# Kernel optimization log

Hardware: AMD Instinct MI355X
Metric: run time of the kernel (lower is better)

The kernel has to match this reference:

```python
import jax, jax.numpy as jnp
import numpy as np

EMBED_DIM = 1024
NUM_HEADS = 16
HEAD_DIM = EMBED_DIM // NUM_HEADS
BATCH = 4
SEQ = 2048


def setup_inputs() -> dict:
    key = jax.random.key(0)
    ks = jax.random.split(key, 5)
    s_in = 1.0 / np.sqrt(EMBED_DIM)
    x = jax.random.normal(ks[0], (BATCH, SEQ, EMBED_DIM), dtype=jnp.float32)
    # torch nn.Linear params: weight [out, in], bias [out]
    qkv_w = jax.random.uniform(ks[1], (3 * EMBED_DIM, EMBED_DIM), jnp.float32, -s_in, s_in)
    qkv_b = jax.random.uniform(ks[2], (3 * EMBED_DIM,), jnp.float32, -s_in, s_in)
    out_w = jax.random.uniform(ks[3], (EMBED_DIM, EMBED_DIM), jnp.float32, -s_in, s_in)
    out_b = jax.random.uniform(ks[4], (EMBED_DIM,), jnp.float32, -s_in, s_in)
    return {"x": x, "qkv_w": qkv_w, "qkv_b": qkv_b, "out_w": out_w, "out_b": out_b}


def reference(x, qkv_w, qkv_b, out_w, out_b):
    B, S, E = x.shape
    qkv = x @ qkv_w.T + qkv_b                      # [B,S,3E]
    qkv = qkv.reshape(B, S, 3, NUM_HEADS, HEAD_DIM)
    qkv = jnp.transpose(qkv, (2, 0, 3, 1, 4))      # [3,B,H,S,D]
    q, k, v = qkv[0], qkv[1], qkv[2]
    scale = jnp.sqrt(jnp.float32(HEAD_DIM))
    scores = jnp.einsum('bhqd,bhkd->bhqk', q, k) / scale  # [B,H,S,S]
    attn = jax.nn.softmax(scores, axis=-1)
    out = jnp.einsum('bhqk,bhkd->bhqd', attn, v)   # [B,H,S,D]
    out = jnp.transpose(out, (0, 2, 1, 3)).reshape(B, S, E)
    return out @ out_w.T + out_b
```

## Files before the change

kernel.cpp:

```cpp
#include <hip/hip_runtime.h>
#include <hip/hip_bf16.h>

typedef _Float16 f16;
typedef __attribute__((ext_vector_type(8))) _Float16 f16x8;
typedef __attribute__((ext_vector_type(4))) _Float16 f16x4;
typedef __attribute__((ext_vector_type(4))) float f32x4;

#define MFMA16(a, b, c) __builtin_amdgcn_mfma_f32_16x16x32_f16(a, b, c, 0, 0, 0)
#define GLDS(src, dst) __builtin_amdgcn_global_load_lds( \
    (const __attribute__((address_space(1))) void*)(src), \
    (__attribute__((address_space(3))) void*)(dst), 16, 0, 0)

__device__ inline unsigned pkrtz(float a, float b) {
    __fp16 __attribute__((ext_vector_type(2))) r = __builtin_amdgcn_cvt_pkrtz(a, b);
    unsigned u; __builtin_memcpy(&u, &r, 4);
    return u;
}
__device__ inline void pl32swap(unsigned& a, unsigned& b) {
    asm volatile("v_permlane32_swap_b32 %0, %1" : "+v"(a), "+v"(b));
}
__device__ inline void pl16swap(unsigned& a, unsigned& b) {
    asm volatile("v_permlane16_swap_b32 %0, %1" : "+v"(a), "+v"(b));
}
__device__ inline float fexp2(float x) {
#if __has_builtin(__builtin_amdgcn_exp2f)
    return __builtin_amdgcn_exp2f(x);
#else
    return exp2f(x);
#endif
}

__global__ void cvt_all(const float4* __restrict__ x, const float4* __restrict__ qw,
                        const float4* __restrict__ ow,
                        f16x4* __restrict__ xo, f16x4* __restrict__ qwo,
                        f16x4* __restrict__ owo) {
    const int N1 = 2097152, N2 = 786432, N3 = 262144;
    int i = blockIdx.x * blockDim.x + threadIdx.x;
    int stride = gridDim.x * blockDim.x;
    for (; i < N1 + N2 + N3; i += stride) {
        const float4* src; f16x4* dst; int j;
        if (i < N1)            { src = x;  dst = xo;  j = i; }
        else if (i < N1 + N2)  { src = qw; dst = qwo; j = i - N1; }
        else                   { src = ow; dst = owo; j = i - N1 - N2; }
        float4 f = src[j];
        f16x4 h;
        h.x = (f16)f.x; h.y = (f16)f.y; h.z = (f16)f.z; h.w = (f16)f.w;
        dst[j] = h;
    }
}

__global__ __launch_bounds__(256, 2) void gemm_bt(
    const f16* __restrict__ A, const f16* __restrict__ Bw,
    const float* __restrict__ bias, int mode,
    f16* __restrict__ qo, f16* __restrict__ ko, f16* __restrict__ vo,
    float* __restrict__ outp)
{
    __shared__ __align__(16) f16 As[128 * 64];
    __shared__ __align__(16) f16 Bs[128 * 64];
    const int tid = threadIdx.x;
    const int wave = tid >> 6, lane = tid & 63;
    const int wr = wave >> 1, wc = wave & 1;
    const int brow = blockIdx.y * 128;
    const int bcol = blockIdx.x * 128;
    const int K = 1024;
    const f16* Ab = A + (size_t)brow * K;
    const f16* Bb = Bw + (size_t)bcol * K;

    const f32x4 fz = {0.0f, 0.0f, 0.0f, 0.0f};
    f32x4 acc[4][4];
#pragma unroll
    for (int m = 0; m < 4; ++m)
#pragma unroll
        for (int n = 0; n < 4; ++n) acc[m][n] = fz;

    const int lrow = lane >> 3;
    const int lcol = (lane & 7) * 8;
    const int cl = lane & 15, rg = lane >> 4;

    for (int k0 = 0; k0 < K; k0 += 64) {
        __syncthreads();
#pragma unroll
        for (int c = 0; c < 4; ++c) {
            const int ch = wave * 4 + c;
            const f16* srcA = Ab + (size_t)(ch * 8 + lrow) * K + k0 + lcol;
            const f16* srcB = Bb + (size_t)(ch * 8 + lrow) * K + k0 + lcol;
            GLDS(srcA, As + ch * 512);
            GLDS(srcB, Bs + ch * 512);
        }
        __syncthreads();
#pragma unroll
        for (int kk = 0; kk < 2; ++kk) {
            f16x8 af[4], bfr[4];
#pragma unroll
            for (int m = 0; m < 4; ++m)
                af[m] = *(const f16x8*)(As + (wr * 64 + m * 16 + cl) * 64 + kk * 32 + rg * 8);
#pragma unroll
            for (int n = 0; n < 4; ++n)
                bfr[n] = *(const f16x8*)(Bs + (wc * 64 + n * 16 + cl) * 64 + kk * 32 + rg * 8);
#pragma unroll
            for (int m = 0; m < 4; ++m)
#pragma unroll
                for (int n = 0; n < 4; ++n)
                    acc[m][n] = MFMA16(af[m], bfr[n], acc[m][n]);
        }
    }

    if (mode == 0) {
#pragma unroll
        for (int n = 0; n < 4; ++n) {
            int col = bcol + wc * 64 + n * 16 + cl;
            float bs = bias[col];
            int which = col >> 10;
            int h = (col & 1023) >> 6;
            int d = col & 63;
            if (which == 2) {
#pragma unroll
                for (int m = 0; m < 4; ++m) {
                    int row0 = brow + wr * 64 + m * 16 + rg * 4;
                    int bb = row0 >> 11, s0 = row0 & 2047;
                    f16x4 pk;
#pragma unroll
                    for (int r = 0; r < 4; ++r) pk[r] = (f16)(acc[m][n][r] + bs);
                    *(f16x4*)(vo + ((size_t)(bb * 16 + h) * 64 + d) * 2048 + s0) = pk;
                }
            } else {
                f16* dst = (which == 0) ? qo : ko;
                float scale = (which == 0) ? 0.125f * 1.44269504f : 1.0f;
#pragma unroll
                for (int m = 0; m < 4; ++m) {
#pragma unroll
                    for (int r = 0; r < 4; ++r) {
                        int row = brow + wr * 64 + m * 16 + rg * 4 + r;
                        int bb = row >> 11, s = row & 2047;
                        dst[((size_t)(bb * 16 + h) * 2048 + s) * 64 + d] =
                            (f16)((acc[m][n][r] + bs) * scale);
                    }
                }
            }
        }
    } else {
#pragma unroll
        for (int n = 0; n < 4; ++n) {
            int col = bcol + wc * 64 + n * 16 + cl;
            float bs = bias[col];
#pragma unroll
            for (int m = 0; m < 4; ++m)
#pragma unroll
                for (int r = 0; r < 4; ++r) {
                    int row = brow + wr * 64 + m * 16 + rg * 4 + r;
                    outp[(size_t)row * 1024 + col] = acc[m][n][r] + bs;
                }
        }
    }
}

__global__ __launch_bounds__(256, 3) void attn_fwd(
    const f16* __restrict__ Q, const f16* __restrict__ Kg,
    const f16* __restrict__ Vtg, f16* __restrict__ Op, float* __restrict__ lp)
{
    const int bid = blockIdx.x;
    const int vid = (bid & 7) * 256 + (bid >> 3);
    const int qx = vid & 15;
    const int bh = (vid >> 4) & 63;
    const int z  = vid >> 10;
    const int q0 = qx * 128;
    const int kb = z * 1024;
    const int tid = threadIdx.x;
    const int wave = tid >> 6, lane = tid & 63;
    const int cl = lane & 15, rg = lane >> 4;
    const f16* Qh = Q + (size_t)bh * 2048 * 64;
    const f16* Kp = Kg + (size_t)bh * 2048 * 64 + (size_t)kb * 64;
    const f16* Vp = Vtg + (size_t)bh * 64 * 2048 + kb;

    __shared__ __align__(16) f16 Ks[2][64 * 64];
    __shared__ __align__(16) f16 Vs[2][64 * 64];

    f16x8 aq[2][2];
#pragma unroll
    for (int m = 0; m < 2; ++m) {
        const f16* qptr = Qh + (size_t)(q0 + wave * 32 + m * 16 + cl) * 64 + rg * 8;
        aq[m][0] = *(const f16x8*)(qptr);
        aq[m][1] = *(const f16x8*)(qptr + 32);
    }

    f16x8 ones8;
#pragma unroll
    for (int j = 0; j < 8; ++j) ones8[j] = (f16)1.0f;

    const int srow0 = tid >> 3;
    const int schunk = tid & 7;
    const int swz = cl & 7;

    const f32x4 fz = {0.0f, 0.0f, 0.0f, 0.0f};
    f32x4 oacc[2][4];
    f32x4 loacc[2];
#pragma unroll
    for (int m = 0; m < 2; ++m) {
        loacc[m] = fz;
#pragma unroll
        for (int da = 0; da < 4; ++da) oacc[m][da] = fz;
    }

#pragma unroll
    for (int c = 0; c < 2; ++c) {
        int row = c * 32 + srow0;
        int sc = (schunk ^ (row & 7)) * 8;
        GLDS(Kp + (size_t)row * 64 + sc,   &Ks[0][(c * 256 + wave * 64) * 8]);
        GLDS(Vp + (size_t)row * 2048 + sc, &Vs[0][(c * 256 + wave * 64) * 8]);
    }

    int cur = 0;
    for (int t = 0; t < 16; ++t) {
        if (t < 15) {
            const int kt = (t + 1) * 64;
#pragma unroll
            for (int c = 0; c < 2; ++c) {
                int row = c * 32 + srow0;
                int sc = (schunk ^ (row & 7)) * 8;
                GLDS(Kp + (size_t)(kt + row) * 64 + sc, &Ks[cur ^ 1][(c * 256 + wave * 64) * 8]);
                GLDS(Vp + (size_t)row * 2048 + kt + sc, &Vs[cur ^ 1][(c * 256 + wave * 64) * 8]);
            }
            asm volatile("s_waitcnt vmcnt(4)" ::: "memory");
        } else {
            asm volatile("s_waitcnt vmcnt(0)" ::: "memory");
        }
        __builtin_amdgcn_sched_barrier(0);
        __builtin_amdgcn_s_barrier();
        __builtin_amdgcn_sched_barrier(0);

        f32x4 sacc[2][4];
        __builtin_amdgcn_s_setprio(1);
#pragma unroll
        for (int fn = 0; fn < 4; ++fn) {
            f16x8 ak0 = *(const f16x8*)(
                &Ks[cur][(fn * 16 + cl) * 64 + (rg ^ swz) * 8]);
            f16x8 ak1 = *(const f16x8*)(
                &Ks[cur][(fn * 16 + cl) * 64 + ((4 | rg) ^ swz) * 8]);
            sacc[0][fn] = MFMA16(ak0, aq[0][0], fz);
            sacc[0][fn] = MFMA16(ak1, aq[0][1], sacc[0][fn]);
            sacc[1][fn] = MFMA16(ak0, aq[1][0], fz);
            sacc[1][fn] = MFMA16(ak1, aq[1][1], sacc[1][fn]);
        }
        __builtin_amdgcn_s_setprio(0);

        f16x8 pbv[2][2];
#pragma unroll
        for (int m = 0; m < 2; ++m) {
            unsigned X0[4], X1[4];
#pragma unroll
            for (int fn = 0; fn < 4; ++fn) {
                float p0 = fexp2(sacc[m][fn][0]);
                float p1 = fexp2(sacc[m][fn][1]);
                float p2 = fexp2(sacc[m][fn][2]);
                float p3 = fexp2(sacc[m][fn][3]);
                X0[fn] = pkrtz(p0, p1);
                X1[fn] = pkrtz(p2, p3);
            }
#pragma unroll
            for (int kk = 0; kk < 2; ++kk) {
                unsigned a0 = X0[2 * kk], b0 = X0[2 * kk + 1];
                unsigned a1 = X1[2 * kk], b1 = X1[2 * kk + 1];
                pl32swap(a0, b0); pl16swap(a0, b0);
                pl32swap(a1, b1); pl16swap(a1, b1);
                unsigned fr[4] = {a0, a1, b0, b1};
                __builtin_memcpy(&pbv[m][kk], fr, 16);
            }
        }

        __builtin_amdgcn_s_setprio(1);
#pragma unroll
        for (int kk = 0; kk < 2; ++kk) {
            loacc[0] = MFMA16(ones8, pbv[0][kk], loacc[0]);
            loacc[1] = MFMA16(ones8, pbv[1][kk], loacc[1]);
#pragma unroll
            for (int da = 0; da < 4; ++da) {
                f16x8 av = *(const f16x8*)(
                    &Vs[cur][(da * 16 + cl) * 64 + (((kk << 2) | rg) ^ swz) * 8]);
                oacc[0][da] = MFMA16(av, pbv[0][kk], oacc[0][da]);
                oacc[1][da] = MFMA16(av, pbv[1][kk], oacc[1][da]);
            }
        }
        __builtin_amdgcn_s_setprio(0);

        asm volatile("s_waitcnt lgkmcnt(0)" ::: "memory");
        __builtin_amdgcn_sched_barrier(0);
        __builtin_amdgcn_s_barrier();
        __builtin_amdgcn_sched_barrier(0);
        cur ^= 1;
    }

    const int bb = bh >> 4, h = bh & 15;
#pragma unroll
    for (int m = 0; m < 2; ++m) {
        int s = q0 + wave * 32 + m * 16 + cl;
        int row = (bb * 2048 + s) * 16 + h;
        f16* op = Op + (size_t)z * 8388608 + (size_t)row * 64;
#pragma unroll
        for (int da = 0; da < 4; ++da) {
            f16x4 ov;
#pragma unroll
            for (int r = 0; r < 4; ++r) ov[r] = (f16)oacc[m][da][r];
            *(f16x4*)(op + da * 16 + rg * 4) = ov;
        }
        if (rg == 0) lp[z * 131072 + row] = loacc[m][0];
    }
}

__global__ __launch_bounds__(256) void attn_merge(
    const f16* __restrict__ Op, const float* __restrict__ lp, f16* __restrict__ AO)
{
    int i = blockIdx.x * 256 + threadIdx.x;
    int row = i >> 3, c = (i & 7) * 8;
    float inv = 1.0f / (lp[row] + lp[row + 131072]);
    f16x8 a = *(const f16x8*)(Op + (size_t)row * 64 + c);
    f16x8 b = *(const f16x8*)(Op + 8388608 + (size_t)row * 64 + c);
    f16x8 o;
#pragma unroll
    for (int j = 0; j < 8; ++j) o[j] = (f16)(((float)a[j] + (float)b[j]) * inv);
    *(f16x8*)(AO + (size_t)row * 64 + c) = o;
}

extern "C" void kernel_launch(void* const* d_in, const int* in_sizes, int n_in,
                              void* d_out, int out_size, void* d_ws, size_t ws_size,
                              hipStream_t stream) {
    const float* x     = (const float*)d_in[0];
    const float* qkv_w = (const float*)d_in[1];
    const float* qkv_b = (const float*)d_in[2];
    const float* out_w = (const float*)d_in[3];
    const float* out_b = (const float*)d_in[4];
    float* out = (float*)d_out;

    char* ws = (char*)d_ws;
    size_t off = 0;
    f16* x_h  = (f16*)(ws + off); off += 16777216;
    f16* qw_h = (f16*)(ws + off); off += 6291456;
    f16* ow_h = (f16*)(ws + off); off += 2097152;
    f16* Qb   = (f16*)(ws + off); off += 16777216;
    f16* Kb   = (f16*)(ws + off); off += 16777216;
    f16* Vb   = (f16*)(ws + off); off += 16777216;
    f16* AO   = (f16*)(ws + off); off += 16777216;
    f16* Opart= (f16*)(ws + off); off += 33554432;
    float* lpart = (float*)(ws + off); off += 1048576;

    cvt_all<<<2048, 256, 0, stream>>>((const float4*)x, (const float4*)qkv_w,
                                      (const float4*)out_w,
                                      (f16x4*)x_h, (f16x4*)qw_h, (f16x4*)ow_h);

    dim3 g1(24, 64);
    gemm_bt<<<g1, dim3(256), 0, stream>>>(x_h, qw_h, qkv_b, 0, Qb, Kb, Vb, nullptr);
    attn_fwd<<<2048, dim3(256), 0, stream>>>(Qb, Kb, Vb, Opart, lpart);
    attn_merge<<<4096, dim3(256), 0, stream>>>(Opart, lpart, AO);
    dim3 g2(8, 64);
    gemm_bt<<<g2, dim3(256), 0, stream>>>(AO, ow_h, out_b, 1, nullptr, nullptr, nullptr, out);
}
```

Before: 196.7 us.

## Use 256x256 double-buffered swizzled GEMM kernel for QKV projection

Replaces the 128x128 QKV projection GEMM with a dedicated 256x256-tile, 512-thread kernel. It double-buffers LDS with async global-to-LDS loads and manual vmcnt waits, XOR-swizzles LDS chunks to avoid bank conflicts, and raises wave priority around the MFMA block. The aim is more operand reuse per load and overlap of loads with compute. The cost is 128KB of LDS, one block per CU, and a smaller grid of 384 blocks that may leave CUs underfilled. The output-projection GEMM is split into its own kernel with unchanged logic.

```diff
diff --git a/kernel.cpp b/kernel.cpp
--- a/kernel.cpp
+++ b/kernel.cpp
@@ -49,11 +49,129 @@
     }
 }
 
-__global__ __launch_bounds__(256, 2) void gemm_bt(
+__global__ __launch_bounds__(512, 1) void gemm256_qkv(
     const f16* __restrict__ A, const f16* __restrict__ Bw,
-    const float* __restrict__ bias, int mode,
-    f16* __restrict__ qo, f16* __restrict__ ko, f16* __restrict__ vo,
-    float* __restrict__ outp)
+    const float* __restrict__ bias,
+    f16* __restrict__ qo, f16* __restrict__ ko, f16* __restrict__ vo)
+{
+    __shared__ __align__(16) f16 As[2][256 * 64];
+    __shared__ __align__(16) f16 Bs[2][256 * 64];
+    const int tid = threadIdx.x;
+    const int wave = tid >> 6, lane = tid & 63;
+    const int wr = wave >> 2, wc = wave & 3;
+    const int brow = blockIdx.y * 256;
+    const int bcol = blockIdx.x * 256;
+    const int K = 1024;
+    const f16* Ab = A + (size_t)brow * K;
+    const f16* Bb = Bw + (size_t)bcol * K;
+
+    const int cl = lane & 15, rg = lane >> 4;
+    const int swz = cl & 7;
+    const int schunk = tid & 7;
+
+    const f32x4 fz = {0.0f, 0.0f, 0.0f, 0.0f};
+    f32x4 acc[8][4];
+#pragma unroll
+    for (int m = 0; m < 8; ++m)
+#pragma unroll
+        for (int n = 0; n < 4; ++n) acc[m][n] = fz;
+
+#define STAGE(b, k0)                                                             \
+    {                                                                            \
+        _Pragma("unroll")                                                        \
+        for (int q = 0; q < 4; ++q) {                                            \
+            int id = q * 512 + tid;                                              \
+            int row = id >> 3;                                                   \
+            int sc = (schunk ^ (row & 7)) * 8;                                   \
+            GLDS(Ab + (size_t)row * 1024 + (k0) + sc, &As[b][id * 8 - lane * 8 + lane * 8]); \
+        }                                                                        \
+        _Pragma("unroll")                                                        \
+        for (int q = 0; q < 4; ++q) {                                            \
+            int id = q * 512 + tid;                                              \
+            int row = id >> 3;                                                   \
+            int sc = (schunk ^ (row & 7)) * 8;                                   \
+            GLDS(Bb + (size_t)row * 1024 + (k0) + sc, &Bs[b][id * 8]);           \
+        }                                                                        \
+    }
+
+    STAGE(0, 0);
+
+    int cur = 0;
+    for (int t = 0; t < 16; ++t) {
+        if (t < 15) {
+            STAGE(cur ^ 1, (t + 1) * 64);
+            asm volatile("s_waitcnt vmcnt(8)" ::: "memory");
+        } else {
+            asm volatile("s_waitcnt vmcnt(0)" ::: "memory");
+        }
+        __builtin_amdgcn_sched_barrier(0);
+        __builtin_amdgcn_s_barrier();
+        __builtin_amdgcn_sched_barrier(0);
+
+        __builtin_amdgcn_s_setprio(1);
+#pragma unroll
+        for (int kk = 0; kk < 2; ++kk) {
+            f16x8 af[8];
+#pragma unroll
+            for (int m = 0; m < 8; ++m)
+                af[m] = *(const f16x8*)(
+                    &As[cur][((wr * 128 + m * 16 + cl) * 8 + (((kk << 2) | rg) ^ swz)) * 8]);
+#pragma unroll
+            for (int n = 0; n < 4; ++n) {
+                f16x8 bf = *(const f16x8*)(
+                    &Bs[cur][((wc * 64 + n * 16 + cl) * 8 + (((kk << 2) | rg) ^ swz)) * 8]);
+#pragma unroll
+                for (int m = 0; m < 8; ++m)
+                    acc[m][n] = MFMA16(af[m], bf, acc[m][n]);
+            }
+        }
+        __builtin_amdgcn_s_setprio(0);
+
+        asm volatile("s_waitcnt lgkmcnt(0)" ::: "memory");
+        __builtin_amdgcn_sched_barrier(0);
+        __builtin_amdgcn_s_barrier();
+        __builtin_amdgcn_sched_barrier(0);
+        cur ^= 1;
+    }
+#undef STAGE
+
+#pragma unroll
+    for (int n = 0; n < 4; ++n) {
+        int col = bcol + wc * 64 + n * 16 + cl;
+        float bs = bias[col];
+        int which = col >> 10;
+        int h = (col & 1023) >> 6;
+        int d = col & 63;
+        if (which == 2) {
+#pragma unroll
+            for (int m = 0; m < 8; ++m) {
+                int row0 = brow + wr * 128 + m * 16 + rg * 4;
+                int bb = row0 >> 11, s0 = row0 & 2047;
+                f16x4 pk;
+#pragma unroll
+                for (int r = 0; r < 4; ++r) pk[r] = (f16)(acc[m][n][r] + bs);
+                *(f16x4*)(vo + ((size_t)(bb * 16 + h) * 64 + d) * 2048 + s0) = pk;
+            }
+        } else {
+            f16* dst = (which == 0) ? qo : ko;
+            float scale = (which == 0) ? 0.125f * 1.44269504f : 1.0f;
+#pragma unroll
+            for (int m = 0; m < 8; ++m) {
+#pragma unroll
+                for (int r = 0; r < 4; ++r) {
+                    int row = brow + wr * 128 + m * 16 + rg * 4 + r;
+                    int bb = row >> 11, s = row & 2047;
+                    dst[((size_t)(bb * 16 + h) * 2048 + s) * 64 + d] =
+                        (f16)((acc[m][n][r] + bs) * scale);
+                }
+            }
+        }
+    }
+}
+
+__global__ __launch_bounds__(256, 2) void gemm_out(
+    const f16* __restrict__ A, const f16* __restrict__ Bw,
+    const float* __restrict__ bias, float* __restrict__ outp)
 {
     __shared__ __align__(16) f16 As[128 * 64];
     __shared__ __align__(16) f16 Bs[128 * 64];
@@ -82,10 +200,8 @@
 #pragma unroll
         for (int c = 0; c < 4; ++c) {
             const int ch = wave * 4 + c;
-            const f16* srcA = Ab + (size_t)(ch * 8 + lrow) * K + k0 + lcol;
-            const f16* srcB = Bb + (size_t)(ch * 8 + lrow) * K + k0 + lcol;
-            GLDS(srcA, As + ch * 512);
-            GLDS(srcB, Bs + ch * 512);
+            GLDS(Ab + (size_t)(ch * 8 + lrow) * K + k0 + lcol, As + ch * 512);
+            GLDS(Bb + (size_t)(ch * 8 + lrow) * K + k0 + lcol, Bs + ch * 512);
         }
         __syncthreads();
 #pragma unroll
@@ -104,53 +220,17 @@
                     acc[m][n] = MFMA16(af[m], bfr[n], acc[m][n]);
         }
     }
-
-    if (mode == 0) {
-#pragma unroll
-        for (int n = 0; n < 4; ++n) {
-            int col = bcol + wc * 64 + n * 16 + cl;
-            float bs = bias[col];
-            int which = col >> 10;
-            int h = (col & 1023) >> 6;
-            int d = col & 63;
-            if (which == 2) {
-#pragma unroll
-                for (int m = 0; m < 4; ++m) {
-                    int row0 = brow + wr * 64 + m * 16 + rg * 4;
-                    int bb = row0 >> 11, s0 = row0 & 2047;
-                    f16x4 pk;
-#pragma unroll
-                    for (int r = 0; r < 4; ++r) pk[r] = (f16)(acc[m][n][r] + bs);
-                    *(f16x4*)(vo + ((size_t)(bb * 16 + h) * 64 + d) * 2048 + s0) = pk;
-                }
-            } else {
-                f16* dst = (which == 0) ? qo : ko;
-                float scale = (which == 0) ? 0.125f * 1.44269504f : 1.0f;
-#pragma unroll
-                for (int m = 0; m < 4; ++m) {
-#pragma unroll
-                    for (int r = 0; r < 4; ++r) {
-                        int row = brow + wr * 64 + m * 16 + rg * 4 + r;
-                        int bb = row >> 11, s = row & 2047;
-                        dst[((size_t)(bb * 16 + h) * 2048 + s) * 64 + d] =
-                            (f16)((acc[m][n][r] + bs) * scale);
-                    }
-                }
-            }
-        }
-    } else {
-#pragma unroll
-        for (int n = 0; n < 4; ++n) {
-            int col = bcol + wc * 64 + n * 16 + cl;
-            float bs = bias[col];
-#pragma unroll
-            for (int m = 0; m < 4; ++m)
-#pragma unroll
-                for (int r = 0; r < 4; ++r) {
-                    int row = brow + wr * 64 + m * 16 + rg * 4 + r;
-                    outp[(size_t)row * 1024 + col] = acc[m][n][r] + bs;
-                }
-        }
+#pragma unroll
+    for (int n = 0; n < 4; ++n) {
+        int col = bcol + wc * 64 + n * 16 + cl;
+        float bs = bias[col];
+#pragma unroll
+        for (int m = 0; m < 4; ++m)
+#pragma unroll
+            for (int r = 0; r < 4; ++r) {
+                int row = brow + wr * 64 + m * 16 + rg * 4 + r;
+                outp[(size_t)row * 1024 + col] = acc[m][n][r] + bs;
+            }
     }
 }
 
@@ -346,10 +426,10 @@
                                       (const float4*)out_w,
                                       (f16x4*)x_h, (f16x4*)qw_h, (f16x4*)ow_h);
 
-    dim3 g1(24, 64);
-    gemm_bt<<<g1, dim3(256), 0, stream>>>(x_h, qw_h, qkv_b, 0, Qb, Kb, Vb, nullptr);
+    dim3 g1(12, 32);
+    gemm256_qkv<<<g1, dim3(512), 0, stream>>>(x_h, qw_h, qkv_b, Qb, Kb, Vb);
     attn_fwd<<<2048, dim3(256), 0, stream>>>(Qb, Kb, Vb, Opart, lpart);
     attn_merge<<<4096, dim3(256), 0, stream>>>(Opart, lpart, AO);
     dim3 g2(8, 64);
-    gemm_bt<<<g2, dim3(256), 0, stream>>>(AO, ow_h, out_b, 1, nullptr, nullptr, nullptr, out);
-}
+    gemm_out<<<g2, dim3(256), 0, stream>>>(AO, ow_h, out_b, out);
+}
```

New measurement: 209.7 us. 6.6% more time.

## Drop split-KV attention and merge kernel; remap GEMM blocks per XCD

Applied to the files above, without the earlier changes.

The attention kernel now runs over the full key length of 2048 in one block per 128 queries, not two 1024-key halves, and applies the softmax normalization in its epilogue. This removes the attn_merge kernel and its partial output buffers. Both GEMM launches switch to a 1D grid with an XCD-aware block remap so neighbouring tiles share L2. The risk is that attention now launches 1024 blocks instead of 2048, so fewer blocks are available to fill the CUs.

```diff
diff --git a/kernel.cpp b/kernel.cpp
--- a/kernel.cpp
+++ b/kernel.cpp
@@ -51,17 +51,19 @@
 
 __global__ __launch_bounds__(256, 2) void gemm_bt(
     const f16* __restrict__ A, const f16* __restrict__ Bw,
-    const float* __restrict__ bias, int mode,
+    const float* __restrict__ bias, int mode, int nbn, int chunk,
     f16* __restrict__ qo, f16* __restrict__ ko, f16* __restrict__ vo,
     float* __restrict__ outp)
 {
     __shared__ __align__(16) f16 As[128 * 64];
     __shared__ __align__(16) f16 Bs[128 * 64];
+    const int bid = blockIdx.x;
+    const int vid = (bid & 7) * chunk + (bid >> 3);
+    const int brow = (vid / nbn) * 128;
+    const int bcol = (vid % nbn) * 128;
     const int tid = threadIdx.x;
     const int wave = tid >> 6, lane = tid & 63;
     const int wr = wave >> 1, wc = wave & 1;
-    const int brow = blockIdx.y * 128;
-    const int bcol = blockIdx.x * 128;
     const int K = 1024;
     const f16* Ab = A + (size_t)brow * K;
     const f16* Bb = Bw + (size_t)bcol * K;
@@ -82,10 +84,8 @@
 #pragma unroll
         for (int c = 0; c < 4; ++c) {
             const int ch = wave * 4 + c;
-            const f16* srcA = Ab + (size_t)(ch * 8 + lrow) * K + k0 + lcol;
-            const f16* srcB = Bb + (size_t)(ch * 8 + lrow) * K + k0 + lcol;
-            GLDS(srcA, As + ch * 512);
-            GLDS(srcB, Bs + ch * 512);
+            GLDS(Ab + (size_t)(ch * 8 + lrow) * K + k0 + lcol, As + ch * 512);
+            GLDS(Bb + (size_t)(ch * 8 + lrow) * K + k0 + lcol, Bs + ch * 512);
         }
         __syncthreads();
 #pragma unroll
@@ -156,21 +156,19 @@
 
 __global__ __launch_bounds__(256, 3) void attn_fwd(
     const f16* __restrict__ Q, const f16* __restrict__ Kg,
-    const f16* __restrict__ Vtg, f16* __restrict__ Op, float* __restrict__ lp)
+    const f16* __restrict__ Vtg, f16* __restrict__ AO)
 {
     const int bid = blockIdx.x;
-    const int vid = (bid & 7) * 256 + (bid >> 3);
+    const int vid = (bid & 7) * 128 + (bid >> 3);
     const int qx = vid & 15;
-    const int bh = (vid >> 4) & 63;
-    const int z  = vid >> 10;
+    const int bh = vid >> 4;
     const int q0 = qx * 128;
-    const int kb = z * 1024;
     const int tid = threadIdx.x;
     const int wave = tid >> 6, lane = tid & 63;
     const int cl = lane & 15, rg = lane >> 4;
     const f16* Qh = Q + (size_t)bh * 2048 * 64;
-    const f16* Kp = Kg + (size_t)bh * 2048 * 64 + (size_t)kb * 64;
-    const f16* Vp = Vtg + (size_t)bh * 64 * 2048 + kb;
+    const f16* Kp = Kg + (size_t)bh * 2048 * 64;
+    const f16* Vp = Vtg + (size_t)bh * 64 * 2048;
 
     __shared__ __align__(16) f16 Ks[2][64 * 64];
     __shared__ __align__(16) f16 Vs[2][64 * 64];
@@ -210,8 +208,8 @@
     }
 
     int cur = 0;
-    for (int t = 0; t < 16; ++t) {
-        if (t < 15) {
+    for (int t = 0; t < 32; ++t) {
+        if (t < 31) {
             const int kt = (t + 1) * 64;
 #pragma unroll
             for (int c = 0; c < 2; ++c) {
@@ -292,32 +290,17 @@
     const int bb = bh >> 4, h = bh & 15;
 #pragma unroll
     for (int m = 0; m < 2; ++m) {
+        float inv = 1.0f / loacc[m][0];
         int s = q0 + wave * 32 + m * 16 + cl;
-        int row = (bb * 2048 + s) * 16 + h;
-        f16* op = Op + (size_t)z * 8388608 + (size_t)row * 64;
+        f16* op = AO + ((size_t)(bb * 2048 + s) * 16 + h) * 64;
 #pragma unroll
         for (int da = 0; da < 4; ++da) {
             f16x4 ov;
 #pragma unroll
-            for (int r = 0; r < 4; ++r) ov[r] = (f16)oacc[m][da][r];
+            for (int r = 0; r < 4; ++r) ov[r] = (f16)(oacc[m][da][r] * inv);
             *(f16x4*)(op + da * 16 + rg * 4) = ov;
         }
-        if (rg == 0) lp[z * 131072 + row] = loacc[m][0];
-    }
-}
-
-__global__ __launch_bounds__(256) void attn_merge(
-    const f16* __restrict__ Op, const float* __restrict__ lp, f16* __restrict__ AO)
-{
-    int i = blockIdx.x * 256 + threadIdx.x;
-    int row = i >> 3, c = (i & 7) * 8;
-    float inv = 1.0f / (lp[row] + lp[row + 131072]);
-    f16x8 a = *(const f16x8*)(Op + (size_t)row * 64 + c);
-    f16x8 b = *(const f16x8*)(Op + 8388608 + (size_t)row * 64 + c);
-    f16x8 o;
-#pragma unroll
-    for (int j = 0; j < 8; ++j) o[j] = (f16)(((float)a[j] + (float)b[j]) * inv);
-    *(f16x8*)(AO + (size_t)row * 64 + c) = o;
+    }
 }
 
 extern "C" void kernel_launch(void* const* d_in, const int* in_sizes, int n_in,
@@ -339,17 +322,14 @@
     f16* Kb   = (f16*)(ws + off); off += 16777216;
     f16* Vb   = (f16*)(ws + off); off += 16777216;
     f16* AO   = (f16*)(ws + off); off += 16777216;
-    f16* Opart= (f16*)(ws + off); off += 33554432;
-    float* lpart = (float*)(ws + off); off += 1048576;
 
     cvt_all<<<2048, 256, 0, stream>>>((const float4*)x, (const float4*)qkv_w,
                                       (const float4*)out_w,
                                       (f16x4*)x_h, (f16x4*)qw_h, (f16x4*)ow_h);
 
-    dim3 g1(24, 64);
-    gemm_bt<<<g1, dim3(256), 0, stream>>>(x_h, qw_h, qkv_b, 0, Qb, Kb, Vb, nullptr);
-    attn_fwd<<<2048, dim3(256), 0, stream>>>(Qb, Kb, Vb, Opart, lpart);
-    attn_merge<<<4096, dim3(256), 0, stream>>>(Opart, lpart, AO);
-    dim3 g2(8, 64);
-    gemm_bt<<<g2, dim3(256), 0, stream>>>(AO, ow_h, out_b, 1, nullptr, nullptr, nullptr, out);
-}
+    gemm_bt<<<1536, dim3(256), 0, stream>>>(x_h, qw_h, qkv_b, 0, 24, 192,
+                                            Qb, Kb, Vb, nullptr);
+    attn_fwd<<<1024, dim3(256), 0, stream>>>(Qb, Kb, Vb, AO);
+    gemm_bt<<<512, dim3(256), 0, stream>>>(AO, ow_h, out_b, 1, 8, 64,
+                                           nullptr, nullptr, nullptr, out);
+}
```

New measurement: 189.2 us. -3.8%, faster.
